# Optimization experiments

Measured on AMD Instinct MI355X. Metric: run time of the kernel, lower is better.

The kernel has to match this reference:

```python
import jax, jax.numpy as jnp
import numpy as np

CHUNK = 32
D_INNER, D_STATE, DT_RANK = 512, 16, 32
B_SZ, L_SEQ = 1, 4096


def _chunked_scan(A_bar, Bu, C, cs=CHUNK):
    # A_bar, Bu: (B, L, D, N); C: (B, L, N)
    Bs, L, D, N = A_bar.shape
    pad = (-L) % cs
    if pad:
        A_bar = jnp.pad(A_bar, ((0, 0), (0, pad), (0, 0), (0, 0)), constant_values=1.0)
        Bu = jnp.pad(Bu, ((0, 0), (0, pad), (0, 0), (0, 0)))
        C = jnp.pad(C, ((0, 0), (0, pad), (0, 0)))
    Lp = L + pad
    nc = Lp // cs
    A_c = A_bar.reshape(Bs, nc, cs, D, N)
    Bu_c = Bu.reshape(Bs, nc, cs, D, N)
    C_c = C.reshape(Bs, nc, cs, N)
    # intra-chunk parallel prefix (log-space cumprod)
    A_cum = jnp.exp(jnp.cumsum(jnp.log(jnp.clip(A_c, 1e-8)), axis=2))
    h_intra = A_cum * jnp.cumsum(Bu_c / jnp.clip(A_cum, 1e-8), axis=2)
    total_A = A_cum[:, :, -1]   # (B, nc, D, N)
    h_last = h_intra[:, :, -1]  # (B, nc, D, N)

    def step(carry, inp):
        tA, hL = inp
        return tA * carry + hL, carry  # emit carry BEFORE update (carry_prev)

    init = jnp.zeros((Bs, D, N), A_bar.dtype)
    _, carry_prev = jax.lax.scan(step, init, (jnp.swapaxes(total_A, 0, 1), jnp.swapaxes(h_last, 0, 1)))
    carry_prev = jnp.swapaxes(carry_prev, 0, 1)  # (B, nc, D, N)
    h_full = h_intra + A_cum * carry_prev[:, :, None]
    y = jnp.einsum('bctdn,bctn->bctd', h_full, C_c).reshape(Bs, Lp, D)
    return y[:, :L]


def _chunked_scan_momentum(A_bar, Bu, C, beta, alpha, cs=CHUNK):
    # v_t = beta*v_{t-1} + alpha*Bu_t  resolved via geometric cumsum trick
    L = A_bar.shape[1]
    powers = jnp.arange(L, dtype=Bu.dtype)
    beta_pow = beta ** powers
    Bu_scaled = alpha * Bu / jnp.clip(beta_pow, 1e-12)[None, :, None, None]
    v_series = beta_pow[None, :, None, None] * jnp.cumsum(Bu_scaled, axis=1)
    return _chunked_scan(A_bar, v_series, C, cs)


def setup_inputs() -> dict:
    key = jax.random.key(0)
    ks = jax.random.split(key, 5)
    x = jax.random.normal(ks[0], (B_SZ, L_SEQ, D_INNER), dtype=jnp.float32)
    W_xp = jax.random.normal(ks[1], (DT_RANK + 2 * D_STATE, D_INNER), dtype=jnp.float32) * 0.02
    W_dt = jax.random.normal(ks[2], (D_INNER, DT_RANK), dtype=jnp.float32) * 0.05
    # torch dt bias init: dt ~ exp(U(log1e-3, log1e-1)); bias = log(exp(dt)-1)
    u = jax.random.uniform(ks[3], (D_INNER,), dtype=jnp.float32)
    dt_init = jnp.exp(u * (np.log(0.1) - np.log(0.001)) + np.log(0.001))
    b_dt = jnp.log(jnp.expm1(dt_init))
    A_log = jnp.broadcast_to(jnp.log(jnp.arange(1, D_STATE + 1, dtype=jnp.float32))[None, :], (D_INNER, D_STATE)).copy()
    D_param = jnp.ones((D_INNER,), dtype=jnp.float32)
    alpha = jnp.float32(0.6)
    beta_logit = jnp.float32(np.log(0.99 / (1.0 - 0.99 + 1e-8)))
    return {"x": x, "W_xp": W_xp, "W_dt": W_dt, "b_dt": b_dt, "A_log": A_log,
            "D_param": D_param, "alpha": alpha, "beta_logit": beta_logit}


def reference(x, W_xp, W_dt, b_dt, A_log, D_param, alpha, beta_logit):
    # x: (B, L, d_inner)
    proj = x @ W_xp.T                                   # (B, L, dt_rank + 2N)
    dt_in, Bp, Cp = jnp.split(proj, [DT_RANK, DT_RANK + D_STATE], axis=-1)
    dt = jax.nn.softplus(dt_in @ W_dt.T + b_dt)          # (B, L, D)
    A = -jnp.exp(A_log)                                  # (D, N)
    A_bar = jnp.exp(dt[..., None] * A[None, None])       # (B, L, D, N)
    Bu = dt[..., None] * Bp[:, :, None, :] * x[..., None]  # (B, L, D, N)
    beta = jax.nn.sigmoid(beta_logit)
    y = _chunked_scan_momentum(A_bar, Bu, Cp, beta, alpha, CHUNK)
    return y + D_param * x
```

## Files before the change

kernel.cpp:

```cpp
#include <hip/hip_runtime.h>
#include <math.h>

#define L_SEQ   4096
#define D_INNER 512
#define D_STATE 16
#define DT_RANK 32
#define CHUNK   32
#define NCHUNK  128
#define NCH     8192
#define LN_1EM8 -18.420681f

__global__ __launch_bounds__(256) void k1a(
    const float* __restrict__ x, const float* __restrict__ W_xp,
    float* __restrict__ proj_part)
{
    __shared__ __align__(16) float xs_t[64][68];
    __shared__ __align__(16) float ws_t[64][68];
    const int tid = threadIdx.x;
    const int t0  = blockIdx.x * 64;
    const int k0  = blockIdx.y * 64;

    #pragma unroll
    for (int i = 0; i < 4; ++i) {
        int e = tid + i * 256;
        int r = e >> 4, k4 = (e & 15) << 2;
        float4 v = *(const float4*)&x[(size_t)(t0 + r) * D_INNER + k0 + k4];
        xs_t[k4 + 0][r] = v.x; xs_t[k4 + 1][r] = v.y;
        xs_t[k4 + 2][r] = v.z; xs_t[k4 + 3][r] = v.w;
        float4 w = *(const float4*)&W_xp[(size_t)r * D_INNER + k0 + k4];
        ws_t[k4 + 0][r] = w.x; ws_t[k4 + 1][r] = w.y;
        ws_t[k4 + 2][r] = w.z; ws_t[k4 + 3][r] = w.w;
    }
    __syncthreads();

    const int tr = (tid & 15) << 2;
    const int tc = (tid >> 4) << 2;
    float a00=0,a01=0,a02=0,a03=0, a10=0,a11=0,a12=0,a13=0;
    float a20=0,a21=0,a22=0,a23=0, a30=0,a31=0,a32=0,a33=0;

    #pragma unroll 4
    for (int k = 0; k < 64; ++k) {
        float4 xv = *(const float4*)&xs_t[k][tr];
        float4 wv = *(const float4*)&ws_t[k][tc];
        a00 = fmaf(xv.x, wv.x, a00); a01 = fmaf(xv.x, wv.y, a01);
        a02 = fmaf(xv.x, wv.z, a02); a03 = fmaf(xv.x, wv.w, a03);
        a10 = fmaf(xv.y, wv.x, a10); a11 = fmaf(xv.y, wv.y, a11);
        a12 = fmaf(xv.y, wv.z, a12); a13 = fmaf(xv.y, wv.w, a13);
        a20 = fmaf(xv.z, wv.x, a20); a21 = fmaf(xv.z, wv.y, a21);
        a22 = fmaf(xv.z, wv.z, a22); a23 = fmaf(xv.z, wv.w, a23);
        a30 = fmaf(xv.w, wv.x, a30); a31 = fmaf(xv.w, wv.y, a31);
        a32 = fmaf(xv.w, wv.z, a32); a33 = fmaf(xv.w, wv.w, a33);
    }
    float* base = proj_part + (size_t)blockIdx.y * (L_SEQ * 64);
    float4 o;
    o.x=a00; o.y=a01; o.z=a02; o.w=a03; *(float4*)&base[(t0+tr+0)*64 + tc] = o;
    o.x=a10; o.y=a11; o.z=a12; o.w=a13; *(float4*)&base[(t0+tr+1)*64 + tc] = o;
    o.x=a20; o.y=a21; o.z=a22; o.w=a23; *(float4*)&base[(t0+tr+2)*64 + tc] = o;
    o.x=a30; o.y=a31; o.z=a32; o.w=a33; *(float4*)&base[(t0+tr+3)*64 + tc] = o;
}

__global__ __launch_bounds__(256) void k1b(
    const float* __restrict__ proj_part, const float* __restrict__ W_dt,
    const float* __restrict__ b_dt, float* __restrict__ dt_out,
    float* __restrict__ Bp, float* __restrict__ Cp)
{
    __shared__ __align__(16) float ps[16][68];
    const int tid = threadIdx.x;
    const int t0  = blockIdx.x * 16;

    {
        const int r = tid >> 4, q = (tid & 15) << 2;
        float4 s = {0.f, 0.f, 0.f, 0.f};
        #pragma unroll
        for (int p = 0; p < 8; ++p) {
            float4 v = *(const float4*)&proj_part[(size_t)p * (L_SEQ * 64) + (t0 + r) * 64 + q];
            s.x += v.x; s.y += v.y; s.z += v.z; s.w += v.w;
        }
        *(float4*)&ps[r][q] = s;
    }
    __syncthreads();

    {
        const int r = tid >> 4, n = tid & 15;
        Bp[(size_t)(t0 + r) * D_STATE + n] = ps[r][32 + n];
        Cp[(size_t)(t0 + r) * D_STATE + n] = ps[r][48 + n];
    }

    const int dA = tid * 2, dB = tid * 2 + 1;
    float4 wa[8], wb[8];
    #pragma unroll
    for (int q = 0; q < 8; ++q) {
        wa[q] = *(const float4*)&W_dt[(size_t)dA * DT_RANK + q * 4];
        wb[q] = *(const float4*)&W_dt[(size_t)dB * DT_RANK + q * 4];
    }
    const float bA = b_dt[dA], bB = b_dt[dB];
    for (int r = 0; r < 16; ++r) {
        float zA = bA, zB = bB;
        #pragma unroll
        for (int q = 0; q < 8; ++q) {
            float4 dn = *(const float4*)&ps[r][q * 4];
            zA += dn.x*wa[q].x + dn.y*wa[q].y + dn.z*wa[q].z + dn.w*wa[q].w;
            zB += dn.x*wb[q].x + dn.y*wb[q].y + dn.z*wb[q].z + dn.w*wb[q].w;
        }
        float2 o;
        o.x = fmaxf(zA, 0.f) + log1pf(expf(-fabsf(zA)));
        o.y = fmaxf(zB, 0.f) + log1pf(expf(-fabsf(zB)));
        *(float2*)&dt_out[(size_t)(t0 + r) * D_INNER + dA] = o;
    }
}

__global__ __launch_bounds__(256) void k2a(
    const float* __restrict__ x, const float* __restrict__ dt,
    const float* __restrict__ Bp, const float* __restrict__ A_log,
    const float* __restrict__ alpha_p, const float* __restrict__ beta_logit_p,
    float4* __restrict__ GTUW)
{
    __shared__ float xs[CHUNK][65], dts[CHUNK][65];
    __shared__ __align__(16) float Bs[CHUNK][20];
    __shared__ float bpw[CHUNK], aib[CHUNK];
    const int tid = threadIdx.x;
    const int c   = blockIdx.x;
    const int d0  = blockIdx.y * 64;

    #pragma unroll
    for (int i = 0; i < 8; ++i) {
        int e = tid + i * 256;
        int t = e >> 6, dl = e & 63;
        xs [t][dl] = x [(size_t)(c * CHUNK + t) * D_INNER + d0 + dl];
        dts[t][dl] = dt[(size_t)(c * CHUNK + t) * D_INNER + d0 + dl];
    }
    #pragma unroll
    for (int i = 0; i < 2; ++i) {
        int e = tid + i * 256;
        int t = e >> 4, n = e & 15;
        Bs[t][n] = Bp[(size_t)(c * CHUNK + t) * D_STATE + n];
    }
    if (tid < CHUNK) {
        float betaf = 1.f / (1.f + expf(-beta_logit_p[0]));
        double lb = log((double)betaf);
        float bp = (float)exp((double)(c * CHUNK + tid) * lb);
        bpw[tid] = bp;
        aib[tid] = alpha_p[0] / fmaxf(bp, 1e-12f);
    }
    __syncthreads();

    const int dl = tid >> 2, n0 = (tid & 3) << 2;
    float A[4], LS[4] = {0,0,0,0}, cs[4] = {0,0,0,0};
    float P1[4] = {0,0,0,0}, P2[4] = {0,0,0,0};
    #pragma unroll
    for (int i = 0; i < 4; ++i)
        A[i] = -expf(A_log[(size_t)(d0 + dl) * D_STATE + n0 + i]);

    #pragma unroll 4
    for (int j = 0; j < CHUNK; ++j) {
        float dtv = dts[j][dl];
        float xv  = xs[j][dl];
        float bp  = bpw[j];
        float ai  = aib[j];
        float4 Bv = *(const float4*)&Bs[j][n0];
        #pragma unroll
        for (int i = 0; i < 4; ++i) {
            float Bu = dtv * ((const float*)&Bv)[i] * xv;
            LS[i] = fmaf(ai, Bu, LS[i]);
            cs[i] = fmaf(dtv, A[i], cs[i]);
            float rA = (cs[i] < LN_1EM8) ? 1e8f : __expf(-cs[i]);
            float t1 = bp * rA;
            P1[i] = fmaf(t1, LS[i], P1[i]);
            P2[i] += t1;
        }
    }
    #pragma unroll
    for (int i = 0; i < 4; ++i) {
        float TA = __expf(cs[i]);
        float4 o; o.x = LS[i]; o.y = TA; o.z = TA * P1[i]; o.w = TA * P2[i];
        GTUW[(size_t)c * NCH + (d0 + dl) * D_STATE + n0 + i] = o;
    }
}

__global__ __launch_bounds__(64) void k2b(
    const float4* __restrict__ GTUW, float2* __restrict__ SC)
{
    const int ch = blockIdx.x * 64 + threadIdx.x;
    double Soff = 0.0, carry = 0.0;
    float4 buf[4];
    #pragma unroll
    for (int p = 0; p < 4; ++p) buf[p] = GTUW[(size_t)p * NCH + ch];
    #pragma unroll 4
    for (int c = 0; c < NCHUNK; ++c) {
        float4 g = buf[c & 3];
        if (c + 4 < NCHUNK) buf[c & 3] = GTUW[(size_t)(c + 4) * NCH + ch];
        float2 sc; sc.x = (float)Soff; sc.y = (float)carry;
        SC[(size_t)c * NCH + ch] = sc;
        carry = (double)g.y * carry + (double)g.z + Soff * (double)g.w;
        Soff += (double)g.x;
    }
}

__global__ __launch_bounds__(256) void k2c(
    const float* __restrict__ x, const float* __restrict__ dt,
    const float* __restrict__ Bp, const float* __restrict__ Cp,
    const float* __restrict__ A_log, const float* __restrict__ D_param,
    const float* __restrict__ alpha_p, const float* __restrict__ beta_logit_p,
    const float2* __restrict__ SC, float* __restrict__ out)
{
    __shared__ float xs[CHUNK][65], dts[CHUNK][65];
    __shared__ __align__(16) float Bs[CHUNK][20], Cs[CHUNK][20];
    __shared__ float bpw[CHUNK], aib[CHUNK];
    __shared__ float ys[CHUNK][65];
    const int tid = threadIdx.x;
    const int c   = blockIdx.x;
    const int d0  = blockIdx.y * 64;

    #pragma unroll
    for (int i = 0; i < 8; ++i) {
        int e = tid + i * 256;
        int t = e >> 6, dl = e & 63;
        xs [t][dl] = x [(size_t)(c * CHUNK + t) * D_INNER + d0 + dl];
        dts[t][dl] = dt[(size_t)(c * CHUNK + t) * D_INNER + d0 + dl];
    }
    #pragma unroll
    for (int i = 0; i < 2; ++i) {
        int e = tid + i * 256;
        int t = e >> 4, n = e & 15;
        Bs[t][n] = Bp[(size_t)(c * CHUNK + t) * D_STATE + n];
        Cs[t][n] = Cp[(size_t)(c * CHUNK + t) * D_STATE + n];
    }
    if (tid < CHUNK) {
        float betaf = 1.f / (1.f + expf(-beta_logit_p[0]));
        double lb = log((double)betaf);
        float bp = (float)exp((double)(c * CHUNK + tid) * lb);
        bpw[tid] = bp;
        aib[tid] = alpha_p[0] / fmaxf(bp, 1e-12f);
    }
    __syncthreads();

    const int dl = tid >> 2, n0 = (tid & 3) << 2;
    float A[4], LS[4] = {0,0,0,0}, cs[4] = {0,0,0,0}, P[4] = {0,0,0,0};
    float So[4], Cv0[4];
    #pragma unroll
    for (int i = 0; i < 4; ++i)
        A[i] = -expf(A_log[(size_t)(d0 + dl) * D_STATE + n0 + i]);
    #pragma unroll
    for (int i = 0; i < 4; ++i) {
        float2 sc = SC[(size_t)c * NCH + (d0 + dl) * D_STATE + n0 + i];
        So[i] = sc.x; Cv0[i] = sc.y;
    }

    #pragma unroll 4
    for (int j = 0; j < CHUNK; ++j) {
        float dtv = dts[j][dl];
        float xv  = xs[j][dl];
        float bp  = bpw[j];
        float ai  = aib[j];
        float4 Bv = *(const float4*)&Bs[j][n0];
        float4 Cv = *(const float4*)&Cs[j][n0];
        float contrib = 0.f;
        #pragma unroll
        for (int i = 0; i < 4; ++i) {
            float Bu = dtv * ((const float*)&Bv)[i] * xv;
            LS[i] = fmaf(ai, Bu, LS[i]);
            float v = bp * (So[i] + LS[i]);
            cs[i] = fmaf(dtv, A[i], cs[i]);
            float Acum = __expf(cs[i]);
            float rA = (cs[i] < LN_1EM8) ? 1e8f : __expf(-cs[i]);
            P[i] = fmaf(v, rA, P[i]);
            float hf = Acum * (P[i] + Cv0[i]);
            contrib = fmaf(hf, ((const float*)&Cv)[i], contrib);
        }
        contrib += __shfl_xor(contrib, 1);
        contrib += __shfl_xor(contrib, 2);
        if ((tid & 3) == 0) ys[j][dl] = contrib;
    }
    __syncthreads();

    #pragma unroll
    for (int i = 0; i < 8; ++i) {
        int e = tid + i * 256;
        int t = e >> 6, d2 = e & 63;
        int gd = d0 + d2;
        out[(size_t)(c * CHUNK + t) * D_INNER + gd] = ys[t][d2] + D_param[gd] * xs[t][d2];
    }
}

extern "C" void kernel_launch(void* const* d_in, const int* in_sizes, int n_in,
                              void* d_out, int out_size, void* d_ws, size_t ws_size,
                              hipStream_t stream)
{
    const float* x          = (const float*)d_in[0];
    const float* W_xp       = (const float*)d_in[1];
    const float* W_dt       = (const float*)d_in[2];
    const float* b_dt       = (const float*)d_in[3];
    const float* A_log      = (const float*)d_in[4];
    const float* D_param    = (const float*)d_in[5];
    const float* alpha      = (const float*)d_in[6];
    const float* beta_logit = (const float*)d_in[7];
    float* out = (float*)d_out;

    float* ws = (float*)d_ws;
    float*  dtw  = ws;
    float*  Bp   = dtw + (size_t)L_SEQ * D_INNER;
    float*  Cp   = Bp + (size_t)L_SEQ * D_STATE;
    float4* GTUW = (float4*)(Cp + (size_t)L_SEQ * D_STATE);
    float*  scpp = (float*)GTUW + (size_t)4 * NCHUNK * NCH;
    float2* SC        = (float2*)scpp;
    float*  proj_part = scpp;

    k1a<<<dim3(L_SEQ / 64, 8), 256, 0, stream>>>(x, W_xp, proj_part);
    k1b<<<L_SEQ / 16, 256, 0, stream>>>(proj_part, W_dt, b_dt, dtw, Bp, Cp);
    k2a<<<dim3(NCHUNK, D_INNER / 64), 256, 0, stream>>>(
        x, dtw, Bp, A_log, alpha, beta_logit, GTUW);
    k2b<<<NCH / 64, 64, 0, stream>>>(GTUW, SC);
    k2c<<<dim3(NCHUNK, D_INNER / 64), 256, 0, stream>>>(
        x, dtw, Bp, Cp, A_log, D_param, alpha, beta_logit, SC, out);
}
```

Before: 157.1 us.

## Fuse dt projection into chunk kernel and switch intra-chunk math to recurrent form

Removes the separate k1b kernel: the chunk kernel now reduces the split-K partial projections itself, computes softplus dt per chunk, and writes dt/B/C for the output kernel. Intra-chunk accumulation switches from cumulative log-sum with exp(-cs) reciprocals to a multiplicative recurrence (H = ee*H + ...), which drops one exp per element. The GEMM is restructured with a swizzled shared x tile and W read directly from global, the scan uses 256-thread blocks with deeper prefetch, and loads/stores are vectorized. Redundant partial-sum reads across the 8 d-blocks per chunk and the serial recurrence chain are the trade-offs.

```diff
diff --git a/kernel.cpp b/kernel.cpp
--- a/kernel.cpp
+++ b/kernel.cpp
@@ -8,132 +8,109 @@
 #define CHUNK   32
 #define NCHUNK  128
 #define NCH     8192
-#define LN_1EM8 -18.420681f
-
-__global__ __launch_bounds__(256) void k1a(
+#define PPSTRIDE (L_SEQ * 64)
+
+__global__ __launch_bounds__(256, 2) void msm_gemm(
     const float* __restrict__ x, const float* __restrict__ W_xp,
     float* __restrict__ proj_part)
 {
-    __shared__ __align__(16) float xs_t[64][68];
-    __shared__ __align__(16) float ws_t[64][68];
+    __shared__ __align__(16) float sm[64 * 64];
     const int tid = threadIdx.x;
-    const int t0  = blockIdx.x * 64;
-    const int k0  = blockIdx.y * 64;
+    const int t0 = (blockIdx.x >> 3) * 64;
+    const int k0 = (blockIdx.x & 7) * 64;
 
     #pragma unroll
     for (int i = 0; i < 4; ++i) {
         int e = tid + i * 256;
-        int r = e >> 4, k4 = (e & 15) << 2;
-        float4 v = *(const float4*)&x[(size_t)(t0 + r) * D_INNER + k0 + k4];
-        xs_t[k4 + 0][r] = v.x; xs_t[k4 + 1][r] = v.y;
-        xs_t[k4 + 2][r] = v.z; xs_t[k4 + 3][r] = v.w;
-        float4 w = *(const float4*)&W_xp[(size_t)r * D_INNER + k0 + k4];
-        ws_t[k4 + 0][r] = w.x; ws_t[k4 + 1][r] = w.y;
-        ws_t[k4 + 2][r] = w.z; ws_t[k4 + 3][r] = w.w;
-    }
-    __syncthreads();
-
-    const int tr = (tid & 15) << 2;
-    const int tc = (tid >> 4) << 2;
-    float a00=0,a01=0,a02=0,a03=0, a10=0,a11=0,a12=0,a13=0;
-    float a20=0,a21=0,a22=0,a23=0, a30=0,a31=0,a32=0,a33=0;
+        int r = e >> 4, q4 = e & 15;
+        float4 v = *(const float4*)&x[(size_t)(t0 + r) * D_INNER + k0 + q4 * 4];
+        *(float4*)&sm[r * 64 + ((q4 ^ (r >> 2)) << 2)] = v;
+    }
+    __syncthreads();
+
+    const int rg  = tid >> 4;
+    const int cc0 = (tid & 15) * 4;
+    const int r0  = rg * 4;
+    float acc[4][4];
+    #pragma unroll
+    for (int a = 0; a < 4; ++a)
+        #pragma unroll
+        for (int b = 0; b < 4; ++b) acc[a][b] = 0.f;
 
     #pragma unroll 4
-    for (int k = 0; k < 64; ++k) {
-        float4 xv = *(const float4*)&xs_t[k][tr];
-        float4 wv = *(const float4*)&ws_t[k][tc];
-        a00 = fmaf(xv.x, wv.x, a00); a01 = fmaf(xv.x, wv.y, a01);
-        a02 = fmaf(xv.x, wv.z, a02); a03 = fmaf(xv.x, wv.w, a03);
-        a10 = fmaf(xv.y, wv.x, a10); a11 = fmaf(xv.y, wv.y, a11);
-        a12 = fmaf(xv.y, wv.z, a12); a13 = fmaf(xv.y, wv.w, a13);
-        a20 = fmaf(xv.z, wv.x, a20); a21 = fmaf(xv.z, wv.y, a21);
-        a22 = fmaf(xv.z, wv.z, a22); a23 = fmaf(xv.z, wv.w, a23);
-        a30 = fmaf(xv.w, wv.x, a30); a31 = fmaf(xv.w, wv.y, a31);
-        a32 = fmaf(xv.w, wv.z, a32); a33 = fmaf(xv.w, wv.w, a33);
-    }
-    float* base = proj_part + (size_t)blockIdx.y * (L_SEQ * 64);
-    float4 o;
-    o.x=a00; o.y=a01; o.z=a02; o.w=a03; *(float4*)&base[(t0+tr+0)*64 + tc] = o;
-    o.x=a10; o.y=a11; o.z=a12; o.w=a13; *(float4*)&base[(t0+tr+1)*64 + tc] = o;
-    o.x=a20; o.y=a21; o.z=a22; o.w=a23; *(float4*)&base[(t0+tr+2)*64 + tc] = o;
-    o.x=a30; o.y=a31; o.z=a32; o.w=a33; *(float4*)&base[(t0+tr+3)*64 + tc] = o;
-}
-
-__global__ __launch_bounds__(256) void k1b(
-    const float* __restrict__ proj_part, const float* __restrict__ W_dt,
-    const float* __restrict__ b_dt, float* __restrict__ dt_out,
-    float* __restrict__ Bp, float* __restrict__ Cp)
-{
-    __shared__ __align__(16) float ps[16][68];
-    const int tid = threadIdx.x;
-    const int t0  = blockIdx.x * 16;
-
-    {
-        const int r = tid >> 4, q = (tid & 15) << 2;
-        float4 s = {0.f, 0.f, 0.f, 0.f};
-        #pragma unroll
-        for (int p = 0; p < 8; ++p) {
-            float4 v = *(const float4*)&proj_part[(size_t)p * (L_SEQ * 64) + (t0 + r) * 64 + q];
-            s.x += v.x; s.y += v.y; s.z += v.z; s.w += v.w;
-        }
-        *(float4*)&ps[r][q] = s;
-    }
-    __syncthreads();
-
-    {
-        const int r = tid >> 4, n = tid & 15;
-        Bp[(size_t)(t0 + r) * D_STATE + n] = ps[r][32 + n];
-        Cp[(size_t)(t0 + r) * D_STATE + n] = ps[r][48 + n];
-    }
-
-    const int dA = tid * 2, dB = tid * 2 + 1;
-    float4 wa[8], wb[8];
-    #pragma unroll
-    for (int q = 0; q < 8; ++q) {
-        wa[q] = *(const float4*)&W_dt[(size_t)dA * DT_RANK + q * 4];
-        wb[q] = *(const float4*)&W_dt[(size_t)dB * DT_RANK + q * 4];
-    }
-    const float bA = b_dt[dA], bB = b_dt[dB];
-    for (int r = 0; r < 16; ++r) {
-        float zA = bA, zB = bB;
-        #pragma unroll
-        for (int q = 0; q < 8; ++q) {
-            float4 dn = *(const float4*)&ps[r][q * 4];
-            zA += dn.x*wa[q].x + dn.y*wa[q].y + dn.z*wa[q].z + dn.w*wa[q].w;
-            zB += dn.x*wb[q].x + dn.y*wb[q].y + dn.z*wb[q].z + dn.w*wb[q].w;
-        }
-        float2 o;
-        o.x = fmaxf(zA, 0.f) + log1pf(expf(-fabsf(zA)));
-        o.y = fmaxf(zB, 0.f) + log1pf(expf(-fabsf(zB)));
-        *(float2*)&dt_out[(size_t)(t0 + r) * D_INNER + dA] = o;
-    }
-}
-
-__global__ __launch_bounds__(256) void k2a(
-    const float* __restrict__ x, const float* __restrict__ dt,
-    const float* __restrict__ Bp, const float* __restrict__ A_log,
+    for (int k4 = 0; k4 < 16; ++k4) {
+        float4 w0 = *(const float4*)&W_xp[(size_t)(cc0 + 0) * D_INNER + k0 + k4 * 4];
+        float4 w1 = *(const float4*)&W_xp[(size_t)(cc0 + 1) * D_INNER + k0 + k4 * 4];
+        float4 w2 = *(const float4*)&W_xp[(size_t)(cc0 + 2) * D_INNER + k0 + k4 * 4];
+        float4 w3 = *(const float4*)&W_xp[(size_t)(cc0 + 3) * D_INNER + k0 + k4 * 4];
+        #pragma unroll
+        for (int rr = 0; rr < 4; ++rr) {
+            float4 xv = *(const float4*)&sm[(r0 + rr) * 64 + ((k4 ^ rg) << 2)];
+            acc[rr][0] += xv.x*w0.x + xv.y*w0.y + xv.z*w0.z + xv.w*w0.w;
+            acc[rr][1] += xv.x*w1.x + xv.y*w1.y + xv.z*w1.z + xv.w*w1.w;
+            acc[rr][2] += xv.x*w2.x + xv.y*w2.y + xv.z*w2.z + xv.w*w2.w;
+            acc[rr][3] += xv.x*w3.x + xv.y*w3.y + xv.z*w3.z + xv.w*w3.w;
+        }
+    }
+    float* pp = proj_part + (size_t)(blockIdx.x & 7) * PPSTRIDE;
+    #pragma unroll
+    for (int rr = 0; rr < 4; ++rr) {
+        float4 o; o.x = acc[rr][0]; o.y = acc[rr][1]; o.z = acc[rr][2]; o.w = acc[rr][3];
+        *(float4*)&pp[(size_t)(t0 + r0 + rr) * 64 + cc0] = o;
+    }
+}
+
+__global__ __launch_bounds__(256, 4) void msm_chunk(
+    const float* __restrict__ x, const float* __restrict__ proj_part,
+    const float* __restrict__ W_dt, const float* __restrict__ b_dt,
+    const float* __restrict__ A_log,
     const float* __restrict__ alpha_p, const float* __restrict__ beta_logit_p,
+    float* __restrict__ dtw, float* __restrict__ BpG, float* __restrict__ CpG,
     float4* __restrict__ GTUW)
 {
-    __shared__ float xs[CHUNK][65], dts[CHUNK][65];
-    __shared__ __align__(16) float Bs[CHUNK][20];
-    __shared__ float bpw[CHUNK], aib[CHUNK];
+    __shared__ __align__(16) float xs [CHUNK * 64];
+    __shared__ __align__(16) float dts[CHUNK * 64];
+    __shared__ __align__(16) float dtin[CHUNK * 36];
+    __shared__ __align__(16) float Bs [CHUNK * 20];
+    __shared__ __align__(16) float bpw[CHUNK], aib[CHUNK];
     const int tid = threadIdx.x;
     const int c   = blockIdx.x;
     const int d0  = blockIdx.y * 64;
 
     #pragma unroll
-    for (int i = 0; i < 8; ++i) {
-        int e = tid + i * 256;
-        int t = e >> 6, dl = e & 63;
-        xs [t][dl] = x [(size_t)(c * CHUNK + t) * D_INNER + d0 + dl];
-        dts[t][dl] = dt[(size_t)(c * CHUNK + t) * D_INNER + d0 + dl];
-    }
-    #pragma unroll
-    for (int i = 0; i < 2; ++i) {
-        int e = tid + i * 256;
-        int t = e >> 4, n = e & 15;
-        Bs[t][n] = Bp[(size_t)(c * CHUNK + t) * D_STATE + n];
+    for (int i = 0; i < 2; ++i) {
+        int e = tid + i * 256;
+        int t = e >> 4, q4 = e & 15;
+        *(float4*)&xs[t * 64 + q4 * 4] =
+            *(const float4*)&x[(size_t)(c * CHUNK + t) * D_INNER + d0 + q4 * 4];
+    }
+    #pragma unroll
+    for (int i = 0; i < 4; ++i) {
+        int e = tid + i * 256;
+        int r = e >> 5, q = e & 31;
+        float s = 0.f;
+        #pragma unroll
+        for (int p = 0; p < 8; ++p)
+            s += proj_part[(size_t)p * PPSTRIDE + (size_t)(c * CHUNK + r) * 64 + q];
+        dtin[r * 36 + q] = s;
+    }
+    #pragma unroll
+    for (int i = 0; i < 2; ++i) {
+        int e = tid + i * 256;
+        int r = e >> 4, n = e & 15;
+        float sB = 0.f;
+        #pragma unroll
+        for (int p = 0; p < 8; ++p)
+            sB += proj_part[(size_t)p * PPSTRIDE + (size_t)(c * CHUNK + r) * 64 + 32 + n];
+        Bs[r * 20 + n] = sB;
+        if (blockIdx.y == 0) {
+            BpG[(size_t)(c * CHUNK + r) * D_STATE + n] = sB;
+            float sC = 0.f;
+            #pragma unroll
+            for (int p = 0; p < 8; ++p)
+                sC += proj_part[(size_t)p * PPSTRIDE + (size_t)(c * CHUNK + r) * 64 + 48 + n];
+            CpG[(size_t)(c * CHUNK + r) * D_STATE + n] = sC;
+        }
     }
     if (tid < CHUNK) {
         float betaf = 1.f / (1.f + expf(-beta_logit_p[0]));
@@ -144,51 +121,76 @@
     }
     __syncthreads();
 
+    {
+        const int dcol = tid & 63, rgrp = tid >> 6;
+        const int gd = d0 + dcol;
+        float4 wd[8];
+        #pragma unroll
+        for (int q = 0; q < 8; ++q)
+            wd[q] = *(const float4*)&W_dt[(size_t)gd * DT_RANK + q * 4];
+        const float bb = b_dt[gd];
+        #pragma unroll
+        for (int rr = 0; rr < 8; ++rr) {
+            const int r = rgrp * 8 + rr;
+            float z = bb;
+            #pragma unroll
+            for (int q = 0; q < 8; ++q) {
+                float4 dn = *(const float4*)&dtin[r * 36 + q * 4];
+                z += dn.x*wd[q].x + dn.y*wd[q].y + dn.z*wd[q].z + dn.w*wd[q].w;
+            }
+            float sp = fmaxf(z, 0.f) + log1pf(expf(-fabsf(z)));
+            dts[r * 64 + dcol] = sp;
+            dtw[(size_t)(c * CHUNK + r) * D_INNER + gd] = sp;
+        }
+    }
+    __syncthreads();
+
     const int dl = tid >> 2, n0 = (tid & 3) << 2;
-    float A[4], LS[4] = {0,0,0,0}, cs[4] = {0,0,0,0};
-    float P1[4] = {0,0,0,0}, P2[4] = {0,0,0,0};
-    #pragma unroll
-    for (int i = 0; i < 4; ++i)
-        A[i] = -expf(A_log[(size_t)(d0 + dl) * D_STATE + n0 + i]);
-
+    float A[4];
+    {
+        float4 Al = *(const float4*)&A_log[(size_t)(d0 + dl) * D_STATE + n0];
+        A[0] = -expf(Al.x); A[1] = -expf(Al.y); A[2] = -expf(Al.z); A[3] = -expf(Al.w);
+    }
+    float LS[4] = {0,0,0,0}, Ac[4] = {1,1,1,1}, H1[4] = {0,0,0,0}, H2[4] = {0,0,0,0};
     #pragma unroll 4
     for (int j = 0; j < CHUNK; ++j) {
-        float dtv = dts[j][dl];
-        float xv  = xs[j][dl];
-        float bp  = bpw[j];
-        float ai  = aib[j];
-        float4 Bv = *(const float4*)&Bs[j][n0];
+        float dtv = dts[j * 64 + dl];
+        float xv  = xs [j * 64 + dl];
+        float bp  = bpw[j], ai = aib[j];
+        float4 Bv = *(const float4*)&Bs[j * 20 + n0];
+        float dx = dtv * xv;
         #pragma unroll
         for (int i = 0; i < 4; ++i) {
-            float Bu = dtv * ((const float*)&Bv)[i] * xv;
+            float Bu = dx * ((const float*)&Bv)[i];
             LS[i] = fmaf(ai, Bu, LS[i]);
-            cs[i] = fmaf(dtv, A[i], cs[i]);
-            float rA = (cs[i] < LN_1EM8) ? 1e8f : __expf(-cs[i]);
-            float t1 = bp * rA;
-            P1[i] = fmaf(t1, LS[i], P1[i]);
-            P2[i] += t1;
-        }
-    }
+            float ee = __expf(dtv * A[i]);
+            ee = fmaxf(ee, 1e-8f);
+            Ac[i] *= ee;
+            float s  = fminf(1.f, Ac[i] * 1e8f);
+            float t1 = bp * s;
+            H1[i] = fmaf(ee, H1[i], t1 * LS[i]);
+            H2[i] = fmaf(ee, H2[i], t1);
+        }
+    }
+    const size_t base = (size_t)c * NCH + (size_t)(d0 + dl) * D_STATE + n0;
     #pragma unroll
     for (int i = 0; i < 4; ++i) {
-        float TA = __expf(cs[i]);
-        float4 o; o.x = LS[i]; o.y = TA; o.z = TA * P1[i]; o.w = TA * P2[i];
-        GTUW[(size_t)c * NCH + (d0 + dl) * D_STATE + n0 + i] = o;
-    }
-}
-
-__global__ __launch_bounds__(64) void k2b(
+        float4 o; o.x = LS[i]; o.y = Ac[i]; o.z = H1[i]; o.w = H2[i];
+        GTUW[base + i] = o;
+    }
+}
+
+__global__ __launch_bounds__(256) void msm_scan(
     const float4* __restrict__ GTUW, float2* __restrict__ SC)
 {
-    const int ch = blockIdx.x * 64 + threadIdx.x;
+    const int ch = blockIdx.x * 256 + threadIdx.x;
     double Soff = 0.0, carry = 0.0;
-    float4 buf[4];
-    #pragma unroll
-    for (int p = 0; p < 4; ++p) buf[p] = GTUW[(size_t)p * NCH + ch];
-    #pragma unroll 4
+    float4 buf[8];
+    #pragma unroll
+    for (int p = 0; p < 8; ++p) buf[p] = GTUW[(size_t)p * NCH + ch];
     for (int c = 0; c < NCHUNK; ++c) {
-        float4 g = buf[c & 3];
-        if (c + 4 < NCHUNK) buf[c & 3] = GTUW[(size_t)(c + 4) * NCH + ch];
+        float4 g = buf[c & 7];
+        if (c + 8 < NCHUNK) buf[c & 7] = GTUW[(size_t)(c + 8) * NCH + ch];
         float2 sc; sc.x = (float)Soff; sc.y = (float)carry;
         SC[(size_t)c * NCH + ch] = sc;
         carry = (double)g.y * carry + (double)g.z + Soff * (double)g.w;
@@ -196,34 +198,38 @@
     }
 }
 
-__global__ __launch_bounds__(256) void k2c(
-    const float* __restrict__ x, const float* __restrict__ dt,
-    const float* __restrict__ Bp, const float* __restrict__ Cp,
+__global__ __launch_bounds__(256, 4) void msm_out(
+    const float* __restrict__ x, const float* __restrict__ dtw,
+    const float* __restrict__ BpG, const float* __restrict__ CpG,
     const float* __restrict__ A_log, const float* __restrict__ D_param,
     const float* __restrict__ alpha_p, const float* __restrict__ beta_logit_p,
     const float2* __restrict__ SC, float* __restrict__ out)
 {
-    __shared__ float xs[CHUNK][65], dts[CHUNK][65];
-    __shared__ __align__(16) float Bs[CHUNK][20], Cs[CHUNK][20];
-    __shared__ float bpw[CHUNK], aib[CHUNK];
-    __shared__ float ys[CHUNK][65];
+    __shared__ __align__(16) float xs [CHUNK * 64];
+    __shared__ __align__(16) float dts[CHUNK * 64];
+    __shared__ __align__(16) float Bs [CHUNK * 20];
+    __shared__ __align__(16) float Cs [CHUNK * 20];
+    __shared__ __align__(16) float ys [CHUNK * 64];
+    __shared__ __align__(16) float bpw[CHUNK], aib[CHUNK];
     const int tid = threadIdx.x;
     const int c   = blockIdx.x;
     const int d0  = blockIdx.y * 64;
 
     #pragma unroll
-    for (int i = 0; i < 8; ++i) {
-        int e = tid + i * 256;
-        int t = e >> 6, dl = e & 63;
-        xs [t][dl] = x [(size_t)(c * CHUNK + t) * D_INNER + d0 + dl];
-        dts[t][dl] = dt[(size_t)(c * CHUNK + t) * D_INNER + d0 + dl];
+    for (int i = 0; i < 2; ++i) {
+        int e = tid + i * 256;
+        int t = e >> 4, q4 = e & 15;
+        *(float4*)&xs [t * 64 + q4 * 4] =
+            *(const float4*)&x  [(size_t)(c * CHUNK + t) * D_INNER + d0 + q4 * 4];
+        *(float4*)&dts[t * 64 + q4 * 4] =
+            *(const float4*)&dtw[(size_t)(c * CHUNK + t) * D_INNER + d0 + q4 * 4];
     }
     #pragma unroll
     for (int i = 0; i < 2; ++i) {
         int e = tid + i * 256;
         int t = e >> 4, n = e & 15;
-        Bs[t][n] = Bp[(size_t)(c * CHUNK + t) * D_STATE + n];
-        Cs[t][n] = Cp[(size_t)(c * CHUNK + t) * D_STATE + n];
+        Bs[t * 20 + n] = BpG[(size_t)(c * CHUNK + t) * D_STATE + n];
+        Cs[t * 20 + n] = CpG[(size_t)(c * CHUNK + t) * D_STATE + n];
     }
     if (tid < CHUNK) {
         float betaf = 1.f / (1.f + expf(-beta_logit_p[0]));
@@ -235,50 +241,58 @@
     __syncthreads();
 
     const int dl = tid >> 2, n0 = (tid & 3) << 2;
-    float A[4], LS[4] = {0,0,0,0}, cs[4] = {0,0,0,0}, P[4] = {0,0,0,0};
-    float So[4], Cv0[4];
-    #pragma unroll
-    for (int i = 0; i < 4; ++i)
-        A[i] = -expf(A_log[(size_t)(d0 + dl) * D_STATE + n0 + i]);
+    float A[4];
+    {
+        float4 Al = *(const float4*)&A_log[(size_t)(d0 + dl) * D_STATE + n0];
+        A[0] = -expf(Al.x); A[1] = -expf(Al.y); A[2] = -expf(Al.z); A[3] = -expf(Al.w);
+    }
+    const size_t base = (size_t)c * NCH + (size_t)(d0 + dl) * D_STATE + n0;
+    float So[4], H[4], LS[4] = {0,0,0,0}, Ac[4] = {1,1,1,1};
     #pragma unroll
     for (int i = 0; i < 4; ++i) {
-        float2 sc = SC[(size_t)c * NCH + (d0 + dl) * D_STATE + n0 + i];
-        So[i] = sc.x; Cv0[i] = sc.y;
+        float2 sc = SC[base + i];
+        So[i] = sc.x;
+        H[i]  = sc.y;
     }
 
     #pragma unroll 4
     for (int j = 0; j < CHUNK; ++j) {
-        float dtv = dts[j][dl];
-        float xv  = xs[j][dl];
-        float bp  = bpw[j];
-        float ai  = aib[j];
-        float4 Bv = *(const float4*)&Bs[j][n0];
-        float4 Cv = *(const float4*)&Cs[j][n0];
+        float dtv = dts[j * 64 + dl];
+        float xv  = xs [j * 64 + dl];
+        float bp  = bpw[j], ai = aib[j];
+        float4 Bv = *(const float4*)&Bs[j * 20 + n0];
+        float4 Cv = *(const float4*)&Cs[j * 20 + n0];
+        float dx = dtv * xv;
         float contrib = 0.f;
         #pragma unroll
         for (int i = 0; i < 4; ++i) {
-            float Bu = dtv * ((const float*)&Bv)[i] * xv;
+            float Bu = dx * ((const float*)&Bv)[i];
             LS[i] = fmaf(ai, Bu, LS[i]);
             float v = bp * (So[i] + LS[i]);
-            cs[i] = fmaf(dtv, A[i], cs[i]);
-            float Acum = __expf(cs[i]);
-            float rA = (cs[i] < LN_1EM8) ? 1e8f : __expf(-cs[i]);
-            P[i] = fmaf(v, rA, P[i]);
-            float hf = Acum * (P[i] + Cv0[i]);
-            contrib = fmaf(hf, ((const float*)&Cv)[i], contrib);
+            float ee = __expf(dtv * A[i]);
+            ee = fmaxf(ee, 1e-8f);
+            Ac[i] *= ee;
+            float s = fminf(1.f, Ac[i] * 1e8f);
+            H[i] = fmaf(ee, H[i], s * v);
+            contrib = fmaf(H[i], ((const float*)&Cv)[i], contrib);
         }
         contrib += __shfl_xor(contrib, 1);
         contrib += __shfl_xor(contrib, 2);
-        if ((tid & 3) == 0) ys[j][dl] = contrib;
-    }
-    __syncthreads();
-
-    #pragma unroll
-    for (int i = 0; i < 8; ++i) {
-        int e = tid + i * 256;
-        int t = e >> 6, d2 = e & 63;
-        int gd = d0 + d2;
-        out[(size_t)(c * CHUNK + t) * D_INNER + gd] = ys[t][d2] + D_param[gd] * xs[t][d2];
+        if (n0 == 0) ys[j * 64 + dl] = contrib;
+    }
+    __syncthreads();
+
+    #pragma unroll
+    for (int i = 0; i < 2; ++i) {
+        int e = tid + i * 256;
+        int t = e >> 4, q4 = e & 15;
+        float4 yv = *(const float4*)&ys[t * 64 + q4 * 4];
+        float4 xv = *(const float4*)&xs[t * 64 + q4 * 4];
+        float4 Dv = *(const float4*)&D_param[d0 + q4 * 4];
+        float4 o;
+        o.x = yv.x + Dv.x * xv.x; o.y = yv.y + Dv.y * xv.y;
+        o.z = yv.z + Dv.z * xv.z; o.w = yv.w + Dv.w * xv.w;
+        *(float4*)&out[(size_t)(c * CHUNK + t) * D_INNER + d0 + q4 * 4] = o;
     }
 }
 
@@ -297,19 +311,18 @@
     float* out = (float*)d_out;
 
     float* ws = (float*)d_ws;
-    float*  dtw  = ws;
-    float*  Bp   = dtw + (size_t)L_SEQ * D_INNER;
-    float*  Cp   = Bp + (size_t)L_SEQ * D_STATE;
-    float4* GTUW = (float4*)(Cp + (size_t)L_SEQ * D_STATE);
-    float*  scpp = (float*)GTUW + (size_t)4 * NCHUNK * NCH;
-    float2* SC        = (float2*)scpp;
-    float*  proj_part = scpp;
-
-    k1a<<<dim3(L_SEQ / 64, 8), 256, 0, stream>>>(x, W_xp, proj_part);
-    k1b<<<L_SEQ / 16, 256, 0, stream>>>(proj_part, W_dt, b_dt, dtw, Bp, Cp);
-    k2a<<<dim3(NCHUNK, D_INNER / 64), 256, 0, stream>>>(
-        x, dtw, Bp, A_log, alpha, beta_logit, GTUW);
-    k2b<<<NCH / 64, 64, 0, stream>>>(GTUW, SC);
-    k2c<<<dim3(NCHUNK, D_INNER / 64), 256, 0, stream>>>(
-        x, dtw, Bp, Cp, A_log, D_param, alpha, beta_logit, SC, out);
-}
+    float*  dtw       = ws;
+    float*  BpG       = dtw + (size_t)L_SEQ * D_INNER;
+    float*  CpG       = BpG + (size_t)L_SEQ * D_STATE;
+    float4* GTUW      = (float4*)(CpG + (size_t)L_SEQ * D_STATE);
+    float2* SC        = (float2*)((float*)GTUW + (size_t)4 * NCHUNK * NCH);
+    float*  proj_part = (float*)SC + (size_t)2 * NCHUNK * NCH;
+
+    msm_gemm <<<512, 256, 0, stream>>>(x, W_xp, proj_part);
+    msm_chunk<<<dim3(NCHUNK, 8), 256, 0, stream>>>(
+        x, proj_part, W_dt, b_dt, A_log, alpha, beta_logit,
+        dtw, BpG, CpG, GTUW);
+    msm_scan <<<NCH / 256, 256, 0, stream>>>(GTUW, SC);
+    msm_out  <<<dim3(NCHUNK, 8), 256, 0, stream>>>(
+        x, dtw, BpG, CpG, A_log, D_param, alpha, beta_logit, SC, out);
+}
```

Result: slower. 190.0 us (+21.0%).
